# Performance work log

Hardware: AMD Instinct MI355X
Metric: run time of the kernel (lower is better)

Reference implementation:

```python
import jax, jax.numpy as jnp
import numpy as np

D_MODEL = 1024
D_FEATURE = 64
N_HEADS = D_MODEL // D_FEATURE  # 16


def setup_inputs() -> dict:
    key = jax.random.key(0)
    ks = jax.random.split(key, 11)
    B, S = 2, 2048
    s = 1.0 / np.sqrt(D_MODEL)
    inp = {
        "queries": jax.random.normal(ks[0], (B, S, D_MODEL), dtype=jnp.float32),
        "keys": jax.random.normal(ks[1], (B, S, D_MODEL), dtype=jnp.float32),
        "values": jax.random.normal(ks[2], (B, S, D_MODEL), dtype=jnp.float32),
        # Per-head Q/K/V projection weights stacked over heads: [H, d_model, d_feature]
        "Wq": jax.random.normal(ks[3], (N_HEADS, D_MODEL, D_FEATURE), dtype=jnp.float32) * s,
        "Wk": jax.random.normal(ks[4], (N_HEADS, D_MODEL, D_FEATURE), dtype=jnp.float32) * s,
        "Wv": jax.random.normal(ks[5], (N_HEADS, D_MODEL, D_FEATURE), dtype=jnp.float32) * s,
        "bq": jax.random.normal(ks[6], (N_HEADS, D_FEATURE), dtype=jnp.float32) * 0.01,
        "bk": jax.random.normal(ks[7], (N_HEADS, D_FEATURE), dtype=jnp.float32) * 0.01,
        "bv": jax.random.normal(ks[8], (N_HEADS, D_FEATURE), dtype=jnp.float32) * 0.01,
        # Output projection Linear(d_model, d_model)
        "Wo": jax.random.normal(ks[9], (D_MODEL, D_MODEL), dtype=jnp.float32) * s,
        "bo": jax.random.normal(ks[10], (D_MODEL,), dtype=jnp.float32) * 0.01,
    }
    return inp


def reference(queries, keys, values, Wq, Wk, Wv, bq, bk, bv, Wo, bo):
    # Batched equivalent of the per-head loop: all heads' Q/K/V projections
    # done as single einsums, fused multi-head scaled-dot-product attention,
    # then concat (reshape) + output projection. Dropout is identity (eval).
    scale = 1.0 / jnp.sqrt(jnp.asarray(D_FEATURE, queries.dtype))
    q = jnp.einsum("bsd,hdf->bhsf", queries, Wq) + bq[None, :, None, :]
    k = jnp.einsum("bsd,hdf->bhsf", keys, Wk) + bk[None, :, None, :]
    v = jnp.einsum("bsd,hdf->bhsf", values, Wv) + bv[None, :, None, :]
    scores = jnp.einsum("bhsf,bhtf->bhst", q, k) * scale  # [B,H,S,S]
    attn = jax.nn.softmax(scores, axis=-1)
    out = jnp.einsum("bhst,bhtf->bhsf", attn, v)  # [B,H,S,F]
    B, H, S, F = out.shape
    # torch.cat(heads, dim=2): head outputs laid out contiguously -> (h f)
    out = out.transpose(0, 2, 1, 3).reshape(B, S, H * F)
    return out @ Wo.T + bo  # final Linear(d_model, d_model)
```

## Files before the change

kernel.cpp:

```cpp
#include <hip/hip_runtime.h>
#include <hip/hip_bf16.h>

typedef __bf16 bf16_t;
typedef __bf16 bf16x4 __attribute__((ext_vector_type(4)));
typedef __bf16 bf16x8 __attribute__((ext_vector_type(8)));
typedef float f32x4 __attribute__((ext_vector_type(4)));

#define MFMA16(a, b, c) __builtin_amdgcn_mfma_f32_16x16x32_bf16((a), (b), (c), 0, 0, 0)

typedef __attribute__((address_space(3))) void lds_void;
typedef const __attribute__((address_space(1))) void glob_void;
static __device__ __forceinline__ void gl_lds16(const void* g, void* l) {
    __builtin_amdgcn_global_load_lds((glob_void*)g, (lds_void*)l, 16, 0, 0);
}

__global__ __launch_bounds__(256) void prep(
    const float* __restrict__ Wq, const float* __restrict__ Wk,
    const float* __restrict__ Wv, const float* __restrict__ Wo,
    const float* __restrict__ qin, const float* __restrict__ kin,
    const float* __restrict__ vin,
    bf16_t* __restrict__ WqT, bf16_t* __restrict__ WkT,
    bf16_t* __restrict__ WvT, bf16_t* __restrict__ WoT,
    bf16_t* __restrict__ qb, bf16_t* __restrict__ kb, bf16_t* __restrict__ vb)
{
    const int t = threadIdx.x;
    if (blockIdx.x < 256) {
        __shared__ float tile[64][65];
        const int h = blockIdx.x >> 4, d0 = (blockIdx.x & 15) << 6;
        const float* Ws[3] = {Wq, Wk, Wv};
        bf16_t* Wt[3] = {WqT, WkT, WvT};
        const int r = t >> 4, c4 = (t & 15) << 2;
        for (int s = 0; s < 3; ++s) {
            const float* W = Ws[s] + ((size_t)h << 16);
#pragma unroll
            for (int i = 0; i < 4; ++i) {
                float4 v = *(const float4*)&W[(size_t)(d0 + i * 16 + r) * 64 + c4];
                tile[i * 16 + r][c4 + 0] = v.x; tile[i * 16 + r][c4 + 1] = v.y;
                tile[i * 16 + r][c4 + 2] = v.z; tile[i * 16 + r][c4 + 3] = v.w;
            }
            __syncthreads();
#pragma unroll
            for (int i = 0; i < 4; ++i) {
                int f = i * 16 + r;
                bf16x4 o;
                o[0] = (bf16_t)tile[c4 + 0][f]; o[1] = (bf16_t)tile[c4 + 1][f];
                o[2] = (bf16_t)tile[c4 + 2][f]; o[3] = (bf16_t)tile[c4 + 3][f];
                *(bf16x4*)&Wt[s][(((size_t)(h << 6) + f) << 10) + d0 + c4] = o;
            }
            __syncthreads();
        }
    } else {
        size_t id = (size_t)(blockIdx.x - 256) * 256 + t;
        size_t e = id * 4;
        {
            float4 v = *(const float4*)&qin[e];
            bf16x4 o = {(bf16_t)v.x, (bf16_t)v.y, (bf16_t)v.z, (bf16_t)v.w};
            *(bf16x4*)&qb[e] = o;
        }
        {
            float4 v = *(const float4*)&kin[e];
            bf16x4 o = {(bf16_t)v.x, (bf16_t)v.y, (bf16_t)v.z, (bf16_t)v.w};
            *(bf16x4*)&kb[e] = o;
        }
        {
            float4 v = *(const float4*)&vin[e];
            bf16x4 o = {(bf16_t)v.x, (bf16_t)v.y, (bf16_t)v.z, (bf16_t)v.w};
            *(bf16x4*)&vb[e] = o;
        }
        if (id < 262144) {
            float4 v = *(const float4*)&Wo[e];
            bf16x4 o = {(bf16_t)v.x, (bf16_t)v.y, (bf16_t)v.z, (bf16_t)v.w};
            *(bf16x4*)&WoT[e] = o;
        }
    }
}

static __device__ __forceinline__ void gemm_k1024(
    const bf16_t* __restrict__ A, const bf16_t* __restrict__ B,
    int m0, int n0, bf16_t* As, bf16_t* Bs, f32x4 acc[4][4])
{
    const int tid = threadIdx.x, lane = tid & 63, w = tid >> 6;
    const int m = lane & 15, quad = lane >> 4;
    const int wm = (w >> 1) * 64, wn = (w & 1) * 64;
    const int lrow = lane >> 3, lcol = (lane & 7) * 8;

    for (int kt = 0; kt < 1024; kt += 64) {
#pragma unroll
        for (int i = 0; i < 4; ++i) {
            int chunk = i * 4 + w;
            int row = chunk * 8 + lrow;
            gl_lds16(A + (size_t)(m0 + row) * 1024 + kt + lcol, As + chunk * 512);
            gl_lds16(B + (size_t)(n0 + row) * 1024 + kt + lcol, Bs + chunk * 512);
        }
        __syncthreads();
#pragma unroll
        for (int kc = 0; kc < 2; ++kc) {
            bf16x8 af[4], bfr[4];
#pragma unroll
            for (int x = 0; x < 4; ++x) {
                af[x]  = *(const bf16x8*)&As[(wm + x * 16 + m) * 64 + kc * 32 + quad * 8];
                bfr[x] = *(const bf16x8*)&Bs[(wn + x * 16 + m) * 64 + kc * 32 + quad * 8];
            }
#pragma unroll
            for (int mt = 0; mt < 4; ++mt)
#pragma unroll
                for (int nt = 0; nt < 4; ++nt)
                    acc[mt][nt] = MFMA16(af[mt], bfr[nt], acc[mt][nt]);
        }
        __syncthreads();
    }
}

__global__ __launch_bounds__(256) void gemm_proj(
    const bf16_t* __restrict__ qb, const bf16_t* __restrict__ kb,
    const bf16_t* __restrict__ vb, const bf16_t* __restrict__ WT,
    const float* __restrict__ bq, const float* __restrict__ bk,
    const float* __restrict__ bv,
    bf16_t* __restrict__ Qs, bf16_t* __restrict__ Ksb, bf16_t* __restrict__ Vt)
{
    __shared__ alignas(16) bf16_t As[8192], Bs[8192];
    const int z = blockIdx.z;
    const bf16_t* A = (z == 0) ? qb : (z == 1) ? kb : vb;
    const bf16_t* B = WT + (size_t)z * (1024 * 1024);
    const float* bias = (z == 0) ? bq : (z == 1) ? bk : bv;
    const int m0 = blockIdx.y * 128, n0 = blockIdx.x * 128;

    f32x4 zero = {0.f, 0.f, 0.f, 0.f};
    f32x4 acc[4][4];
#pragma unroll
    for (int i = 0; i < 4; ++i)
#pragma unroll
        for (int j = 0; j < 4; ++j) acc[i][j] = zero;

    gemm_k1024(A, B, m0, n0, As, Bs, acc);

    const int lane = threadIdx.x & 63, w = threadIdx.x >> 6;
    const int m = lane & 15, quad = lane >> 4;
    const int wm = (w >> 1) * 64, wn = (w & 1) * 64;

    if (z == 2) {
#pragma unroll
        for (int mt = 0; mt < 4; ++mt)
#pragma unroll
            for (int nt = 0; nt < 4; ++nt) {
                int col = n0 + wn + nt * 16 + m;
                float bb = bias[col];
                int row0 = m0 + wm + mt * 16 + quad * 4;
                int bi = row0 >> 11, s = row0 & 2047;
                bf16x4 p;
#pragma unroll
                for (int r = 0; r < 4; ++r) p[r] = (bf16_t)(acc[mt][nt][r] + bb);
                *(bf16x4*)&Vt[((size_t)bi * 1024 + col) * 2048 + s] = p;
            }
    } else {
        bf16_t* out = z ? Ksb : Qs;
        float sc = z ? 1.0f : 0.125f;
#pragma unroll
        for (int mt = 0; mt < 4; ++mt)
#pragma unroll
            for (int nt = 0; nt < 4; ++nt) {
                int col = n0 + wn + nt * 16 + m;
                float bb = bias[col];
#pragma unroll
                for (int r = 0; r < 4; ++r) {
                    int row = m0 + wm + mt * 16 + quad * 4 + r;
                    out[(size_t)row * 1024 + col] = (bf16_t)((acc[mt][nt][r] + bb) * sc);
                }
            }
    }
}

__global__ __launch_bounds__(256) void gemm_out(
    const bf16_t* __restrict__ Aos, const bf16_t* __restrict__ WoT,
    const float* __restrict__ bo, float* __restrict__ out)
{
    __shared__ alignas(16) bf16_t As[8192], Bs[8192];
    const int m0 = blockIdx.y * 128, n0 = blockIdx.x * 128;

    f32x4 zero = {0.f, 0.f, 0.f, 0.f};
    f32x4 acc[4][4];
#pragma unroll
    for (int i = 0; i < 4; ++i)
#pragma unroll
        for (int j = 0; j < 4; ++j) acc[i][j] = zero;

    gemm_k1024(Aos, WoT, m0, n0, As, Bs, acc);

    const int lane = threadIdx.x & 63, w = threadIdx.x >> 6;
    const int m = lane & 15, quad = lane >> 4;
    const int wm = (w >> 1) * 64, wn = (w & 1) * 64;
#pragma unroll
    for (int mt = 0; mt < 4; ++mt)
#pragma unroll
        for (int nt = 0; nt < 4; ++nt) {
            int col = n0 + wn + nt * 16 + m;
            float bb = bo[col];
#pragma unroll
            for (int r = 0; r < 4; ++r) {
                int row = m0 + wm + mt * 16 + quad * 4 + r;
                out[(size_t)row * 1024 + col] = acc[mt][nt][r] + bb;
            }
        }
}

__global__ __launch_bounds__(256) void attn2(
    const bf16_t* __restrict__ Qb, const bf16_t* __restrict__ Kb,
    const bf16_t* __restrict__ Vt, bf16_t* __restrict__ Ob)
{
    __shared__ alignas(16) bf16_t Ks[32][72];
    __shared__ alignas(16) bf16_t Vts[64][40];
    __shared__ alignas(16) bf16_t Ps[4][32][40];

    const int tid = threadIdx.x, lane = tid & 63, w = tid >> 6;
    const int m = lane & 15, quad = lane >> 4;
    const int bh = blockIdx.x, b = bh >> 4, h = bh & 15;
    const int q0 = blockIdx.y * 128;
    const size_t base = (size_t)b * 2048 * 1024 + h * 64;
    const size_t vbase = ((size_t)b * 1024 + h * 64) * 2048;

    bf16x8 aq[2][2];
#pragma unroll
    for (int mt = 0; mt < 2; ++mt) {
        const bf16_t* qp = Qb + base + (size_t)(q0 + w * 32 + mt * 16 + m) * 1024;
        aq[mt][0] = *(const bf16x8*)(qp + quad * 8);
        aq[mt][1] = *(const bf16x8*)(qp + 32 + quad * 8);
    }
    bf16x8 onesf;
#pragma unroll
    for (int j = 0; j < 8; ++j) onesf[j] = (bf16_t)1.0f;

    f32x4 zero = {0.f, 0.f, 0.f, 0.f};
    f32x4 acc[2][5];
#pragma unroll
    for (int mt = 0; mt < 2; ++mt)
#pragma unroll
        for (int i = 0; i < 5; ++i) acc[mt][i] = zero;

    const int kkey = tid >> 3, kfo = (tid & 7) * 8;
    const int vf = tid >> 2, vko = (tid & 3) * 8;

    bf16x8 rk = *(const bf16x8*)(Kb + base + (size_t)kkey * 1024 + kfo);
    bf16x8 rv = *(const bf16x8*)(Vt + vbase + (size_t)vf * 2048 + vko);

    for (int kt = 0; kt < 2048; kt += 32) {
        *(bf16x8*)&Ks[kkey][kfo] = rk;
        *(bf16x8*)&Vts[vf][vko] = rv;
        __syncthreads();
        if (kt + 32 < 2048) {
            rk = *(const bf16x8*)(Kb + base + (size_t)(kt + 32 + kkey) * 1024 + kfo);
            rv = *(const bf16x8*)(Vt + vbase + (size_t)vf * 2048 + kt + 32 + vko);
        }

        f32x4 s[2][2];
#pragma unroll
        for (int nt = 0; nt < 2; ++nt) {
            bf16x8 b0 = *(const bf16x8*)&Ks[nt * 16 + m][quad * 8];
            bf16x8 b1 = *(const bf16x8*)&Ks[nt * 16 + m][32 + quad * 8];
#pragma unroll
            for (int mt = 0; mt < 2; ++mt) {
                f32x4 t = MFMA16(aq[mt][0], b0, zero);
                t = MFMA16(aq[mt][1], b1, t);
                s[mt][nt] = t;
            }
        }

#pragma unroll
        for (int mt = 0; mt < 2; ++mt)
#pragma unroll
            for (int nt = 0; nt < 2; ++nt)
#pragma unroll
                for (int r = 0; r < 4; ++r)
                    Ps[w][mt * 16 + quad * 4 + r][nt * 16 + m] =
                        (bf16_t)__expf(s[mt][nt][r]);

        bf16x8 ap[2];
#pragma unroll
        for (int mt = 0; mt < 2; ++mt)
            ap[mt] = *(const bf16x8*)&Ps[w][mt * 16 + m][quad * 8];

#pragma unroll
        for (int ft = 0; ft < 4; ++ft) {
            bf16x8 bv = *(const bf16x8*)&Vts[ft * 16 + m][quad * 8];
#pragma unroll
            for (int mt = 0; mt < 2; ++mt)
                acc[mt][ft] = MFMA16(ap[mt], bv, acc[mt][ft]);
        }
#pragma unroll
        for (int mt = 0; mt < 2; ++mt)
            acc[mt][4] = MFMA16(ap[mt], onesf, acc[mt][4]);
        __syncthreads();
    }

#pragma unroll
    for (int mt = 0; mt < 2; ++mt)
#pragma unroll
        for (int r = 0; r < 4; ++r) {
            float inv = __builtin_amdgcn_rcpf(acc[mt][4][r]);
            int row = q0 + w * 32 + mt * 16 + quad * 4 + r;
            bf16_t* op = Ob + base + (size_t)row * 1024;
#pragma unroll
            for (int ft = 0; ft < 4; ++ft)
                op[ft * 16 + m] = (bf16_t)(acc[mt][ft][r] * inv);
        }
}

extern "C" void kernel_launch(void* const* d_in, const int* in_sizes, int n_in,
                              void* d_out, int out_size, void* d_ws, size_t ws_size,
                              hipStream_t stream)
{
    const float* queries = (const float*)d_in[0];
    const float* keys    = (const float*)d_in[1];
    const float* values  = (const float*)d_in[2];
    const float* Wq = (const float*)d_in[3];
    const float* Wk = (const float*)d_in[4];
    const float* Wv = (const float*)d_in[5];
    const float* bq = (const float*)d_in[6];
    const float* bk = (const float*)d_in[7];
    const float* bv = (const float*)d_in[8];
    const float* Wo = (const float*)d_in[9];
    const float* bo = (const float*)d_in[10];

    char* ws = (char*)d_ws;
    const size_t MB = 1024 * 1024;
    bf16_t* WqT = (bf16_t*)(ws + 0 * MB);
    bf16_t* WkT = (bf16_t*)(ws + 2 * MB);
    bf16_t* WvT = (bf16_t*)(ws + 4 * MB);
    bf16_t* WoT = (bf16_t*)(ws + 6 * MB);
    bf16_t* qb  = (bf16_t*)(ws + 8 * MB);
    bf16_t* kb  = (bf16_t*)(ws + 16 * MB);
    bf16_t* vb  = (bf16_t*)(ws + 24 * MB);
    bf16_t* Vt  = (bf16_t*)(ws + 32 * MB);
    bf16_t* Qs  = (bf16_t*)d_out;
    bf16_t* Ksb = (bf16_t*)((char*)d_out + 8 * MB);
    bf16_t* Os  = qb;
    (void)WkT; (void)WvT;

    prep<<<4352, 256, 0, stream>>>(Wq, Wk, Wv, Wo, queries, keys, values,
                                   WqT, WkT, WvT, WoT, qb, kb, vb);

    gemm_proj<<<dim3(8, 32, 3), 256, 0, stream>>>(qb, kb, vb, WqT, bq, bk, bv,
                                                  Qs, Ksb, Vt);

    attn2<<<dim3(32, 16), 256, 0, stream>>>(Qs, Ksb, Vt, Os);

    gemm_out<<<dim3(8, 32), 256, 0, stream>>>(Os, WoT, bo, (float*)d_out);
}
```

Measured before the change: 249.8 us.

## Keep softmax probabilities in registers via transposed QK MFMA and fp16 PV

The attention kernel now computes S^T by swapping the MFMA operands, so each lane holds exp values in the layout the fp16 16x16x16 MFMA expects. This removes the per-wave LDS round trip for P, and V is stored as fp16 to match. The Q scale folds in log2(e) so the cheaper exp2 can be used, and K/V LDS tiles are double-buffered, which drops one barrier per iteration. The output GEMM also switches to 128x64 tiles to launch more blocks, and the attention grid order is swapped. fp16 P and V keep accuracy, since unnormalized exp stays bounded here.

```diff
diff --git a/kernel.cpp b/kernel.cpp
--- a/kernel.cpp
+++ b/kernel.cpp
@@ -4,9 +4,15 @@
 typedef __bf16 bf16_t;
 typedef __bf16 bf16x4 __attribute__((ext_vector_type(4)));
 typedef __bf16 bf16x8 __attribute__((ext_vector_type(8)));
+typedef _Float16 f16_t;
+typedef _Float16 f16x4 __attribute__((ext_vector_type(4)));
+typedef _Float16 f16x8 __attribute__((ext_vector_type(8)));
 typedef float f32x4 __attribute__((ext_vector_type(4)));
 
-#define MFMA16(a, b, c) __builtin_amdgcn_mfma_f32_16x16x32_bf16((a), (b), (c), 0, 0, 0)
+#define MFMA16(a, b, c)  __builtin_amdgcn_mfma_f32_16x16x32_bf16((a), (b), (c), 0, 0, 0)
+#define MFMA16H(a, b, c) __builtin_amdgcn_mfma_f32_16x16x16f16((a), (b), (c), 0, 0, 0)
+
+#define QSCALE 0.18033688089869237f
 
 typedef __attribute__((address_space(3))) void lds_void;
 typedef const __attribute__((address_space(1))) void glob_void;
@@ -116,7 +122,7 @@
     const bf16_t* __restrict__ vb, const bf16_t* __restrict__ WT,
     const float* __restrict__ bq, const float* __restrict__ bk,
     const float* __restrict__ bv,
-    bf16_t* __restrict__ Qs, bf16_t* __restrict__ Ksb, bf16_t* __restrict__ Vt)
+    bf16_t* __restrict__ Qs, bf16_t* __restrict__ Ksb, f16_t* __restrict__ Vt)
 {
     __shared__ alignas(16) bf16_t As[8192], Bs[8192];
     const int z = blockIdx.z;
@@ -147,14 +153,14 @@
                 float bb = bias[col];
                 int row0 = m0 + wm + mt * 16 + quad * 4;
                 int bi = row0 >> 11, s = row0 & 2047;
-                bf16x4 p;
-#pragma unroll
-                for (int r = 0; r < 4; ++r) p[r] = (bf16_t)(acc[mt][nt][r] + bb);
-                *(bf16x4*)&Vt[((size_t)bi * 1024 + col) * 2048 + s] = p;
+                f16x4 p;
+#pragma unroll
+                for (int r = 0; r < 4; ++r) p[r] = (f16_t)(acc[mt][nt][r] + bb);
+                *(f16x4*)&Vt[((size_t)bi * 1024 + col) * 2048 + s] = p;
             }
     } else {
         bf16_t* out = z ? Ksb : Qs;
-        float sc = z ? 1.0f : 0.125f;
+        float sc = z ? 1.0f : QSCALE;
 #pragma unroll
         for (int mt = 0; mt < 4; ++mt)
 #pragma unroll
@@ -174,25 +180,52 @@
     const bf16_t* __restrict__ Aos, const bf16_t* __restrict__ WoT,
     const float* __restrict__ bo, float* __restrict__ out)
 {
-    __shared__ alignas(16) bf16_t As[8192], Bs[8192];
-    const int m0 = blockIdx.y * 128, n0 = blockIdx.x * 128;
+    __shared__ alignas(16) bf16_t As[128 * 64], Bs[64 * 64];
+    const int tid = threadIdx.x, lane = tid & 63, w = tid >> 6;
+    const int m = lane & 15, quad = lane >> 4;
+    const int wm = (w >> 1) * 64, wn = (w & 1) * 32;
+    const int m0 = blockIdx.y * 128, n0 = blockIdx.x * 64;
+    const int lrow = lane >> 3, lcol = (lane & 7) * 8;
 
     f32x4 zero = {0.f, 0.f, 0.f, 0.f};
-    f32x4 acc[4][4];
-#pragma unroll
-    for (int i = 0; i < 4; ++i)
-#pragma unroll
-        for (int j = 0; j < 4; ++j) acc[i][j] = zero;
-
-    gemm_k1024(Aos, WoT, m0, n0, As, Bs, acc);
-
-    const int lane = threadIdx.x & 63, w = threadIdx.x >> 6;
-    const int m = lane & 15, quad = lane >> 4;
-    const int wm = (w >> 1) * 64, wn = (w & 1) * 64;
+    f32x4 acc[4][2];
+#pragma unroll
+    for (int i = 0; i < 4; ++i) { acc[i][0] = zero; acc[i][1] = zero; }
+
+    for (int kt = 0; kt < 1024; kt += 64) {
+#pragma unroll
+        for (int i = 0; i < 4; ++i) {
+            int chunk = i * 4 + w;
+            gl_lds16(Aos + (size_t)(m0 + chunk * 8 + lrow) * 1024 + kt + lcol, As + chunk * 512);
+        }
+#pragma unroll
+        for (int i = 0; i < 2; ++i) {
+            int chunk = i * 4 + w;
+            gl_lds16(WoT + (size_t)(n0 + chunk * 8 + lrow) * 1024 + kt + lcol, Bs + chunk * 512);
+        }
+        __syncthreads();
+#pragma unroll
+        for (int kc = 0; kc < 2; ++kc) {
+            bf16x8 af[4], bfr[2];
+#pragma unroll
+            for (int x = 0; x < 4; ++x)
+                af[x] = *(const bf16x8*)&As[(wm + x * 16 + m) * 64 + kc * 32 + quad * 8];
+#pragma unroll
+            for (int x = 0; x < 2; ++x)
+                bfr[x] = *(const bf16x8*)&Bs[(wn + x * 16 + m) * 64 + kc * 32 + quad * 8];
+#pragma unroll
+            for (int mt = 0; mt < 4; ++mt)
+#pragma unroll
+                for (int nt = 0; nt < 2; ++nt)
+                    acc[mt][nt] = MFMA16(af[mt], bfr[nt], acc[mt][nt]);
+        }
+        __syncthreads();
+    }
+
 #pragma unroll
     for (int mt = 0; mt < 4; ++mt)
 #pragma unroll
-        for (int nt = 0; nt < 4; ++nt) {
+        for (int nt = 0; nt < 2; ++nt) {
             int col = n0 + wn + nt * 16 + m;
             float bb = bo[col];
 #pragma unroll
@@ -203,104 +236,101 @@
         }
 }
 
-__global__ __launch_bounds__(256) void attn2(
+__global__ __launch_bounds__(256) void attn3(
     const bf16_t* __restrict__ Qb, const bf16_t* __restrict__ Kb,
-    const bf16_t* __restrict__ Vt, bf16_t* __restrict__ Ob)
-{
-    __shared__ alignas(16) bf16_t Ks[32][72];
-    __shared__ alignas(16) bf16_t Vts[64][40];
-    __shared__ alignas(16) bf16_t Ps[4][32][40];
+    const f16_t* __restrict__ Vt, bf16_t* __restrict__ Ob)
+{
+    __shared__ alignas(16) bf16_t Ks[2][32][72];
+    __shared__ alignas(16) f16_t  Vts[2][64][40];
 
     const int tid = threadIdx.x, lane = tid & 63, w = tid >> 6;
     const int m = lane & 15, quad = lane >> 4;
-    const int bh = blockIdx.x, b = bh >> 4, h = bh & 15;
-    const int q0 = blockIdx.y * 128;
+    const int bh = blockIdx.y, b = bh >> 4, h = bh & 15;
+    const int q0 = blockIdx.x * 128;
     const size_t base = (size_t)b * 2048 * 1024 + h * 64;
     const size_t vbase = ((size_t)b * 1024 + h * 64) * 2048;
 
     bf16x8 aq[2][2];
 #pragma unroll
-    for (int mt = 0; mt < 2; ++mt) {
-        const bf16_t* qp = Qb + base + (size_t)(q0 + w * 32 + mt * 16 + m) * 1024;
-        aq[mt][0] = *(const bf16x8*)(qp + quad * 8);
-        aq[mt][1] = *(const bf16x8*)(qp + 32 + quad * 8);
-    }
-    bf16x8 onesf;
-#pragma unroll
-    for (int j = 0; j < 8; ++j) onesf[j] = (bf16_t)1.0f;
+    for (int qt = 0; qt < 2; ++qt) {
+        const bf16_t* qp = Qb + base + (size_t)(q0 + w * 32 + qt * 16 + m) * 1024;
+        aq[qt][0] = *(const bf16x8*)(qp + quad * 8);
+        aq[qt][1] = *(const bf16x8*)(qp + 32 + quad * 8);
+    }
+    f16x4 onesh;
+#pragma unroll
+    for (int j = 0; j < 4; ++j) onesh[j] = (f16_t)1.0f;
 
     f32x4 zero = {0.f, 0.f, 0.f, 0.f};
     f32x4 acc[2][5];
 #pragma unroll
-    for (int mt = 0; mt < 2; ++mt)
-#pragma unroll
-        for (int i = 0; i < 5; ++i) acc[mt][i] = zero;
+    for (int qt = 0; qt < 2; ++qt)
+#pragma unroll
+        for (int i = 0; i < 5; ++i) acc[qt][i] = zero;
 
     const int kkey = tid >> 3, kfo = (tid & 7) * 8;
     const int vf = tid >> 2, vko = (tid & 3) * 8;
 
     bf16x8 rk = *(const bf16x8*)(Kb + base + (size_t)kkey * 1024 + kfo);
-    bf16x8 rv = *(const bf16x8*)(Vt + vbase + (size_t)vf * 2048 + vko);
-
+    f16x8  rv = *(const f16x8*)(Vt + vbase + (size_t)vf * 2048 + vko);
+
+    int buf = 0;
     for (int kt = 0; kt < 2048; kt += 32) {
-        *(bf16x8*)&Ks[kkey][kfo] = rk;
-        *(bf16x8*)&Vts[vf][vko] = rv;
+        *(bf16x8*)&Ks[buf][kkey][kfo] = rk;
+        *(f16x8*)&Vts[buf][vf][vko] = rv;
         __syncthreads();
         if (kt + 32 < 2048) {
             rk = *(const bf16x8*)(Kb + base + (size_t)(kt + 32 + kkey) * 1024 + kfo);
-            rv = *(const bf16x8*)(Vt + vbase + (size_t)vf * 2048 + kt + 32 + vko);
+            rv = *(const f16x8*)(Vt + vbase + (size_t)vf * 2048 + kt + 32 + vko);
         }
 
         f32x4 s[2][2];
 #pragma unroll
-        for (int nt = 0; nt < 2; ++nt) {
-            bf16x8 b0 = *(const bf16x8*)&Ks[nt * 16 + m][quad * 8];
-            bf16x8 b1 = *(const bf16x8*)&Ks[nt * 16 + m][32 + quad * 8];
-#pragma unroll
-            for (int mt = 0; mt < 2; ++mt) {
-                f32x4 t = MFMA16(aq[mt][0], b0, zero);
-                t = MFMA16(aq[mt][1], b1, t);
-                s[mt][nt] = t;
-            }
-        }
-
-#pragma unroll
-        for (int mt = 0; mt < 2; ++mt)
-#pragma unroll
-            for (int nt = 0; nt < 2; ++nt)
+        for (int kl = 0; kl < 2; ++kl) {
+            bf16x8 a0 = *(const bf16x8*)&Ks[buf][kl * 16 + m][quad * 8];
+            bf16x8 a1 = *(const bf16x8*)&Ks[buf][kl * 16 + m][32 + quad * 8];
+#pragma unroll
+            for (int qt = 0; qt < 2; ++qt) {
+                f32x4 t = MFMA16(a0, aq[qt][0], zero);
+                s[kl][qt] = MFMA16(a1, aq[qt][1], t);
+            }
+        }
+
+        f16x4 p[2][2];
+#pragma unroll
+        for (int qt = 0; qt < 2; ++qt)
+#pragma unroll
+            for (int kl = 0; kl < 2; ++kl)
 #pragma unroll
                 for (int r = 0; r < 4; ++r)
-                    Ps[w][mt * 16 + quad * 4 + r][nt * 16 + m] =
-                        (bf16_t)__expf(s[mt][nt][r]);
-
-        bf16x8 ap[2];
-#pragma unroll
-        for (int mt = 0; mt < 2; ++mt)
-            ap[mt] = *(const bf16x8*)&Ps[w][mt * 16 + m][quad * 8];
-
-#pragma unroll
-        for (int ft = 0; ft < 4; ++ft) {
-            bf16x8 bv = *(const bf16x8*)&Vts[ft * 16 + m][quad * 8];
-#pragma unroll
-            for (int mt = 0; mt < 2; ++mt)
-                acc[mt][ft] = MFMA16(ap[mt], bv, acc[mt][ft]);
-        }
-#pragma unroll
-        for (int mt = 0; mt < 2; ++mt)
-            acc[mt][4] = MFMA16(ap[mt], onesf, acc[mt][4]);
-        __syncthreads();
-    }
-
-#pragma unroll
-    for (int mt = 0; mt < 2; ++mt)
+                    p[qt][kl][r] = (f16_t)__builtin_amdgcn_exp2f(s[kl][qt][r]);
+
+#pragma unroll
+        for (int kl = 0; kl < 2; ++kl) {
+#pragma unroll
+            for (int ft = 0; ft < 4; ++ft) {
+                f16x4 bv = *(const f16x4*)&Vts[buf][ft * 16 + m][kl * 16 + quad * 4];
+#pragma unroll
+                for (int qt = 0; qt < 2; ++qt)
+                    acc[qt][ft] = MFMA16H(p[qt][kl], bv, acc[qt][ft]);
+            }
+#pragma unroll
+            for (int qt = 0; qt < 2; ++qt)
+                acc[qt][4] = MFMA16H(p[qt][kl], onesh, acc[qt][4]);
+        }
+        buf ^= 1;
+    }
+
+#pragma unroll
+    for (int qt = 0; qt < 2; ++qt)
 #pragma unroll
         for (int r = 0; r < 4; ++r) {
-            float inv = __builtin_amdgcn_rcpf(acc[mt][4][r]);
-            int row = q0 + w * 32 + mt * 16 + quad * 4 + r;
+            float inv = __builtin_amdgcn_rcpf(acc[qt][4][r]);
+            int row = q0 + w * 32 + qt * 16 + quad * 4 + r;
             bf16_t* op = Ob + base + (size_t)row * 1024;
 #pragma unroll
             for (int ft = 0; ft < 4; ++ft)
-                op[ft * 16 + m] = (bf16_t)(acc[mt][ft][r] * inv);
+                op[ft * 16 + m] = (bf16_t)(acc[qt][ft][r] * inv);
         }
 }
 
@@ -329,7 +359,7 @@
     bf16_t* qb  = (bf16_t*)(ws + 8 * MB);
     bf16_t* kb  = (bf16_t*)(ws + 16 * MB);
     bf16_t* vb  = (bf16_t*)(ws + 24 * MB);
-    bf16_t* Vt  = (bf16_t*)(ws + 32 * MB);
+    f16_t*  Vt  = (f16_t*)(ws + 32 * MB);
     bf16_t* Qs  = (bf16_t*)d_out;
     bf16_t* Ksb = (bf16_t*)((char*)d_out + 8 * MB);
     bf16_t* Os  = qb;
@@ -341,7 +371,7 @@
     gemm_proj<<<dim3(8, 32, 3), 256, 0, stream>>>(qb, kb, vb, WqT, bq, bk, bv,
                                                   Qs, Ksb, Vt);
 
-    attn2<<<dim3(32, 16), 256, 0, stream>>>(Qs, Ksb, Vt, Os);
-
-    gemm_out<<<dim3(8, 32), 256, 0, stream>>>(Os, WoT, bo, (float*)d_out);
-}
+    attn3<<<dim3(16, 32), 256, 0, stream>>>(Qs, Ksb, Vt, Os);
+
+    gemm_out<<<dim3(16, 32), 256, 0, stream>>>(Os, WoT, bo, (float*)d_out);
+}
```

New measurement: 240.8 us. 1.04x faster.
